# Kernel tuning notes

Measured on AMD Instinct MI355X. Metric: run time of the kernel, lower is better.

Reference implementation:

```python
import jax, jax.numpy as jnp
import numpy as np

APP_DIM = 27
FEA_PE = 6
VIEW_PE = 6
FEATURE_C = 128
DENSITY_SHIFT = -10.0
DISTANCE_SCALE = 25.0
IN_MLPC = 2 * VIEW_PE * 3 + 2 * FEA_PE * APP_DIM + 3 + APP_DIM  # 390


def positional_encoding(x, freqs):
    # x: [..., C] -> [..., 2*freqs*C]
    freq_bands = (2.0 ** jnp.arange(freqs)).astype(x.dtype)
    pts = (x[..., None] * freq_bands).reshape(x.shape[:-1] + (freqs * x.shape[-1],))
    return jnp.concatenate([jnp.sin(pts), jnp.cos(pts)], axis=-1)


def alpha2weights(alpha):
    # alpha: [N_rays, N_samples]; last sample forced opaque (as in source)
    alpha = alpha.at[:, -1].set(1.0)
    trans = jnp.concatenate(
        [jnp.ones((alpha.shape[0], 1), alpha.dtype), 1.0 - alpha + 1e-10], axis=-1)
    T = jnp.cumprod(trans, axis=-1)
    weights = alpha * T[:, :-1]
    return weights, T


def setup_inputs() -> dict:
    key = jax.random.key(0)
    ks = jax.random.split(key, 12)
    N_rays, N_samples = 4096, 128
    sigma_feat = jax.random.normal(ks[0], (N_rays, N_samples), jnp.float32)
    app_features = 0.1 * jax.random.normal(ks[1], (N_rays, N_samples, APP_DIM), jnp.float32)
    vd = jax.random.normal(ks[2], (N_rays, N_samples, 3), jnp.float32)
    viewdirs = vd / (jnp.linalg.norm(vd, axis=-1, keepdims=True) + 1e-8)
    dists = 0.02 * jax.random.uniform(ks[3], (N_rays, N_samples), jnp.float32)

    def linear(k, fan_in, fan_out):
        kw, kb = jax.random.split(k)
        lim = 1.0 / np.sqrt(fan_in)
        W = jax.random.uniform(kw, (fan_in, fan_out), jnp.float32, -lim, lim)
        b = jax.random.uniform(kb, (fan_out,), jnp.float32, -lim, lim)
        return W, b

    W1, b1 = linear(ks[4], IN_MLPC, FEATURE_C)
    W2, b2 = linear(ks[5], FEATURE_C, FEATURE_C)
    W3, _ = linear(ks[6], FEATURE_C, 3)
    b3 = jnp.zeros((3,), jnp.float32)  # bias of last layer initialized to 0 in source
    return {"sigma_feat": sigma_feat, "app_features": app_features,
            "viewdirs": viewdirs, "dists": dists,
            "W1": W1, "b1": b1, "W2": W2, "b2": b2, "W3": W3, "b3": b3}


def reference(sigma_feat, app_features, viewdirs, dists, W1, b1, W2, b2, W3, b3):
    # feature2density: softplus with density_shift
    sigma = jax.nn.softplus(sigma_feat + DENSITY_SHIFT)
    alpha = 1.0 - jnp.exp(-sigma * dists * DISTANCE_SCALE)  # [N_rays, N_samples]
    weights, _T = alpha2weights(alpha)

    # MLPRender_Fea: cat[features, viewdirs, PE(features), PE(viewdirs)]
    mlp_in = jnp.concatenate(
        [app_features, viewdirs,
         positional_encoding(app_features, FEA_PE),
         positional_encoding(viewdirs, VIEW_PE)], axis=-1)  # [R, S, 390]
    h = jax.nn.relu(jnp.einsum('rsc,cf->rsf', mlp_in, W1) + b1)
    h = jax.nn.relu(jnp.einsum('rsf,fg->rsg', h, W2) + b2)
    rgb = jax.nn.sigmoid(jnp.einsum('rsg,go->rso', h, W3) + b3)  # [R, S, 3]

    rgb_map = jnp.sum(weights[..., None] * rgb, axis=-2)  # [R, 3]
    return rgb_map
```

## Files before the change

kernel.cpp:

```cpp
#include <hip/hip_runtime.h>
#include <math.h>

typedef unsigned short u16;
using bf16x8 = __attribute__((ext_vector_type(8))) short;
using f32x4  = __attribute__((ext_vector_type(4))) float;

#define NS      128
#define NBLOCKS 4096
#define NSLICE  19

#define POOLSZ 32768
#define OH2    16384

#define BAR() do { asm volatile("s_waitcnt lgkmcnt(0)" ::: "memory");        \
                   __builtin_amdgcn_s_barrier();                              \
                   asm volatile("" ::: "memory"); } while (0)

#define MF(A,B,C) __builtin_amdgcn_mfma_f32_16x16x32_bf16((A),(B),(C),0,0,0)

__device__ __forceinline__ u16 f2bf(float f) {
    unsigned int i = __float_as_uint(f);
    return (u16)((i + 0x7FFFu + ((i >> 16) & 1u)) >> 16);
}

__device__ __forceinline__ unsigned pk(float hi, float lo) {
    unsigned r;
    asm("v_cvt_pk_bf16_f32 %0, %1, %2" : "=v"(r) : "v"(lo), "v"(hi));
    return r;
}

__device__ __forceinline__ int afoff_h(int m, int k) {
    int chunk = ((k >> 5) * 8 + (m >> 4)) * 64 + ((k >> 3) & 3) * 16 + (m & 15);
    chunk ^= (k >> 3) & 3;
    return chunk * 8 + (k & 7);
}

__device__ __forceinline__ int orig_k(int ch, int slot) {
    if (ch < 27) {
        if (slot == 0) return ch;
        if (slot <= 6) return 30 + ch * 6 + (slot - 1);
        return 192 + ch * 6 + (slot - 7);
    } else {
        int c = ch - 27;
        if (slot == 0) return 27 + c;
        if (slot <= 6) return 354 + c * 6 + (slot - 1);
        return 372 + c * 6 + (slot - 7);
    }
}

__device__ __forceinline__ float ldch(const float* ap, const float* vp, int c) {
    return (c < 27) ? ap[c] : vp[c - 27];
}

__device__ __forceinline__ void build_x(u16* dst, float v) {
    float rev = v * 0.15915494309189535f;
    rev -= floorf(rev);
    float s0 = __builtin_amdgcn_sinf(rev);
    float c0 = __builtin_amdgcn_cosf(rev);
    float s1 = 2.f * s0 * c0, c1 = c0 * c0 - s0 * s0;
    float s2 = 2.f * s1 * c1, c2 = c1 * c1 - s1 * s1;
    float s3 = 2.f * s2 * c2, c3 = c2 * c2 - s2 * s2;
    float s4 = 2.f * s3 * c3, c4 = c3 * c3 - s3 * s3;
    float s5 = 2.f * s4 * c4, c5 = c4 * c4 - s4 * s4;
    uint4 lo, hi;
    lo.x = pk(s0, v);  lo.y = pk(s2, s1);  lo.z = pk(s4, s3);  lo.w = pk(c0, s5);
    hi.x = pk(c2, c1); hi.y = pk(c4, c3);  hi.z = pk(0.f, c5); hi.w = 0u;
    *(uint4*)(dst)       = lo;
    *(uint4*)(dst + 128) = hi;
}

__global__ __launch_bounds__(256) void prep_kernel(
    const float* __restrict__ W1, const float* __restrict__ W2,
    const float* __restrict__ W3, u16* __restrict__ ws,
    float* __restrict__ out)
{
    int idx = blockIdx.x * 256 + threadIdx.x;
    if (idx < 12288) out[idx] = 0.f;
    if (idx < 61440) {
        int j = idx & 7, lane = (idx >> 3) & 63, nt = (idx >> 9) & 7, ks = idx >> 12;
        int q = lane >> 4, l15 = lane & 15;
        int klocal = q * 8 + j;
        int ch = ks * 2 + (klocal >> 4);
        int slot = klocal & 15;
        int n = nt * 16 + l15;
        ws[idx] = (slot < 13) ? f2bf(W1[orig_k(ch, slot) * 128 + n]) : (u16)0;
    } else if (idx < 77824) {
        int i2 = idx - 61440;
        int j = i2 & 7, lane = (i2 >> 3) & 63, nt = (i2 >> 9) & 7, ks = i2 >> 12;
        int k = ks * 32 + (lane >> 4) * 8 + j;
        int n = nt * 16 + (lane & 15);
        ws[idx] = f2bf(W2[k * 128 + n]);
    } else if (idx < 79872) {
        int i3 = idx - 77824;
        int j = i3 & 7, lane = (i3 >> 3) & 63, ks = i3 >> 9;
        int k = ks * 32 + (lane >> 4) * 8 + j;
        int n = lane & 15;
        ws[idx] = (n < 3) ? f2bf(W3[k * 3 + n]) : (u16)0;
    }
}

#define LOADB2(N0, N1, s)                                                     \
    if ((s) < NSLICE) {                                                       \
        const u16* wp = wp0 + (s) * 4096;                                     \
        N0 = *(const bf16x8*)(wp);                                            \
        N1 = *(const bf16x8*)(wp + 512);                                      \
    }

#define BODYX(s, C0,C1, N0,N1)                                                \
  {                                                                           \
    LOADB2(N0, N1, (s)+2);                                                    \
    const u16* ab = pool + ((s)&7)*4096 + (wm*256 + lane)*8;                  \
    bf16x8 a0 = *(const bf16x8*)(ab);                                         \
    bf16x8 a1 = *(const bf16x8*)(ab + 512);                                   \
    __builtin_amdgcn_s_setprio(1);                                            \
    acc[0][0]=MF(a0,C0,acc[0][0]); acc[0][1]=MF(a0,C1,acc[0][1]);             \
    acc[1][0]=MF(a1,C0,acc[1][0]); acc[1][1]=MF(a1,C1,acc[1][1]);             \
    a0 = *(const bf16x8*)(ab + 1024);                                         \
    a1 = *(const bf16x8*)(ab + 1536);                                         \
    acc[2][0]=MF(a0,C0,acc[2][0]); acc[2][1]=MF(a0,C1,acc[2][1]);             \
    acc[3][0]=MF(a1,C0,acc[3][0]); acc[3][1]=MF(a1,C1,acc[3][1]);             \
    __builtin_amdgcn_s_setprio(0);                                            \
  }

#define BODYX0(s, C0,C1, N0,N1)                                               \
  {                                                                           \
    LOADB2(N0, N1, (s)+2);                                                    \
    const u16* ab = pool + ((s)&7)*4096 + (wm*256 + lane)*8;                  \
    bf16x8 a0 = *(const bf16x8*)(ab);                                         \
    bf16x8 a1 = *(const bf16x8*)(ab + 512);                                   \
    __builtin_amdgcn_s_setprio(1);                                            \
    acc[0][0]=MF(a0,C0,vzero); acc[0][1]=MF(a0,C1,vzero);                     \
    acc[1][0]=MF(a1,C0,vzero); acc[1][1]=MF(a1,C1,vzero);                     \
    a0 = *(const bf16x8*)(ab + 1024);                                         \
    a1 = *(const bf16x8*)(ab + 1536);                                         \
    acc[2][0]=MF(a0,C0,vzero); acc[2][1]=MF(a0,C1,vzero);                     \
    acc[3][0]=MF(a1,C0,vzero); acc[3][1]=MF(a1,C1,vzero);                     \
    __builtin_amdgcn_s_setprio(0);                                            \
  }

#define BODYH(s, C0,C1, N0,N1)                                                \
  {                                                                           \
    LOADB2(N0, N1, (s)+2);                                                    \
    int cb = ((((s)-15)*512) + wm*256 + lane) ^ quad;                         \
    bf16x8 a0 = *(const bf16x8*)(pool + cb*8);                                \
    bf16x8 a1 = *(const bf16x8*)(pool + (cb+64)*8);                           \
    __builtin_amdgcn_s_setprio(1);                                            \
    acc[0][0]=MF(a0,C0,acc[0][0]); acc[0][1]=MF(a0,C1,acc[0][1]);             \
    acc[1][0]=MF(a1,C0,acc[1][0]); acc[1][1]=MF(a1,C1,acc[1][1]);             \
    a0 = *(const bf16x8*)(pool + (cb+128)*8);                                 \
    a1 = *(const bf16x8*)(pool + (cb+192)*8);                                 \
    acc[2][0]=MF(a0,C0,acc[2][0]); acc[2][1]=MF(a0,C1,acc[2][1]);             \
    acc[3][0]=MF(a1,C0,acc[3][0]); acc[3][1]=MF(a1,C1,acc[3][1]);             \
    __builtin_amdgcn_s_setprio(0);                                            \
  }

#define BODYH0(s, C0,C1, N0,N1)                                               \
  {                                                                           \
    LOADB2(N0, N1, (s)+2);                                                    \
    int cb = ((((s)-15)*512) + wm*256 + lane) ^ quad;                         \
    bf16x8 a0 = *(const bf16x8*)(pool + cb*8);                                \
    bf16x8 a1 = *(const bf16x8*)(pool + (cb+64)*8);                           \
    __builtin_amdgcn_s_setprio(1);                                            \
    acc[0][0]=MF(a0,C0,vzero); acc[0][1]=MF(a0,C1,vzero);                     \
    acc[1][0]=MF(a1,C0,vzero); acc[1][1]=MF(a1,C1,vzero);                     \
    a0 = *(const bf16x8*)(pool + (cb+128)*8);                                 \
    a1 = *(const bf16x8*)(pool + (cb+192)*8);                                 \
    acc[2][0]=MF(a0,C0,vzero); acc[2][1]=MF(a0,C1,vzero);                     \
    acc[3][0]=MF(a1,C0,vzero); acc[3][1]=MF(a1,C1,vzero);                     \
    __builtin_amdgcn_s_setprio(0);                                            \
  }

#define GENDQ(p)                                                              \
  {                                                                           \
    if (8*(p)+8  + cl < 30)                                                   \
        build_x(pool + ((2*(p)+2)&3)*8192 + (cl>>1)*4096 + bxoff, pv_a);      \
    if (8*(p)+12 + cl < 30)                                                   \
        build_x(pool + ((2*(p)+3)&3)*8192 + (cl>>1)*4096 + bxoff, pv_b);      \
    pv_a = pv_c; pv_b = pv_d;                                                 \
    if (8*(p)+24 + cl < 30) pv_c = ldch(ap, vp, 8*(p)+24 + cl);               \
    if (8*(p)+28 + cl < 30) pv_d = ldch(ap, vp, 8*(p)+28 + cl);               \
    BAR();                                                                    \
  }

#define EPI4(OFS, ACC, BB, rwb, col)                                          \
  { f32x4 t_ = ACC + BB;                                                      \
    t_ = __builtin_elementwise_max(t_, vzero);                                \
    unsigned w01_ = pk(t_[1], t_[0]);                                         \
    unsigned w23_ = pk(t_[3], t_[2]);                                         \
    pool[(OFS) + afoff_h((rwb) + 0, col)] = (u16)w01_;                        \
    pool[(OFS) + afoff_h((rwb) + 1, col)] = (u16)(w01_ >> 16);                \
    pool[(OFS) + afoff_h((rwb) + 2, col)] = (u16)w23_;                        \
    pool[(OFS) + afoff_h((rwb) + 3, col)] = (u16)(w23_ >> 16); }

__global__ __launch_bounds__(512, 4) void render_kernel(
    const float* __restrict__ sigma_g, const float* __restrict__ app_g,
    const float* __restrict__ view_g,  const float* __restrict__ dists_g,
    const float* __restrict__ b1_g,    const float* __restrict__ b2_g,
    const float* __restrict__ b3_g,    const u16* __restrict__ ws,
    float* __restrict__ out_g)
{
    __shared__ __align__(16) u16 pool[POOLSZ];
    __shared__ __align__(16) float part[NS * 3];
    __shared__ float scanS;

    const int tid  = threadIdx.x;
    const int lane = tid & 63;
    const int wave = tid >> 6;
    const int l15  = lane & 15;
    const int quad = lane >> 4;
    const int wm   = wave >> 2;
    const int wn   = wave & 3;

    const int r  = blockIdx.x;
    const int rb = r * NS;
    const int row = tid & 127;
    const int cl  = tid >> 7;
    const float* ap = app_g  + (rb + row) * 27;
    const float* vp = view_g + (rb + row) * 3;
    const int bxoff = (row >> 4) * 512 + (((cl & 1) * 32) + (row & 15)) * 8;

    const u16* wp0 = ws + (wn * 128 + lane) * 8;
    bf16x8 bP0, bP1, bQ0, bQ1, bR0, bR1;
    LOADB2(bP0, bP1, 0);
    LOADB2(bQ0, bQ1, 1);

    float pv_a = ldch(ap, vp, cl);
    float pv_b = ldch(ap, vp, 4 + cl);
    float pv_c = ldch(ap, vp, 8 + cl);
    float pv_d = ldch(ap, vp, 12 + cl);

    float alpha = 0.f, prod = 1.f, wr = 0.f;
    if (tid < NS) {
        float x  = sigma_g[rb + tid] - 10.f;
        float sp = (x > 20.f) ? x : log1pf(expf(x));
        alpha = 1.f - expf(-sp * dists_g[rb + tid] * 25.f);
        if (tid == NS - 1) alpha = 1.f;
        float tb = 1.f - alpha + 1e-10f;
        prod = tb;
        #pragma unroll
        for (int d = 1; d < 64; d <<= 1) {
            float v = __shfl_up(prod, d);
            if (lane >= d) prod *= v;
        }
        if (tid == 63) scanS = prod;
    }

    build_x(pool +        (cl >> 1) * 4096 + bxoff, pv_a);
    build_x(pool + 8192 + (cl >> 1) * 4096 + bxoff, pv_b);
    pv_a = pv_c; pv_b = pv_d;
    pv_c = ldch(ap, vp, 16 + cl);
    pv_d = ldch(ap, vp, 20 + cl);
    BAR();

    if (tid < NS) {
        float prev = __shfl_up(prod, 1);
        float base = (lane == 0) ? 1.f : prev;
        float scale = (wave == 1) ? scanS : 1.f;
        wr = alpha * base * scale;
    }

    const f32x4 vzero = {0.f, 0.f, 0.f, 0.f};
    f32x4 acc[4][2];

    BODYX0(0, bP0,bP1, bR0,bR1);
    BODYX(1,  bQ0,bQ1, bP0,bP1);
    BODYX(2,  bR0,bR1, bQ0,bQ1);
    BODYX(3,  bP0,bP1, bR0,bR1);  GENDQ(0);
    BODYX(4,  bQ0,bQ1, bP0,bP1);
    BODYX(5,  bR0,bR1, bQ0,bQ1);
    BODYX(6,  bP0,bP1, bR0,bR1);
    BODYX(7,  bQ0,bQ1, bP0,bP1);  GENDQ(1);
    BODYX(8,  bR0,bR1, bQ0,bQ1);
    BODYX(9,  bP0,bP1, bR0,bR1);
    BODYX(10, bQ0,bQ1, bP0,bP1);
    BODYX(11, bR0,bR1, bQ0,bQ1);  GENDQ(2);
    const float b1r0 = b1_g[wn * 32 + l15];
    const float b1r1 = b1_g[wn * 32 + 16 + l15];
    BODYX(12, bP0,bP1, bR0,bR1);
    BODYX(13, bQ0,bQ1, bP0,bP1);
    BODYX(14, bR0,bR1, bQ0,bQ1);

    {
        const f32x4 bb0 = {b1r0, b1r0, b1r0, b1r0};
        const f32x4 bb1 = {b1r1, b1r1, b1r1, b1r1};
        #pragma unroll
        for (int mt = 0; mt < 4; ++mt) {
            int rwb = wm * 64 + mt * 16 + quad * 4;
            EPI4(0, acc[mt][0], bb0, rwb, wn * 32 + l15);
            EPI4(0, acc[mt][1], bb1, rwb, wn * 32 + 16 + l15);
        }
    }
    BAR();

    const float b2r0 = b2_g[wn * 32 + l15];
    const float b2r1 = b2_g[wn * 32 + 16 + l15];

    BODYH0(15, bP0,bP1, bR0,bR1);
    BODYH(16, bQ0,bQ1, bP0,bP1);
    BODYH(17, bR0,bR1, bQ0,bQ1);
    BODYH(18, bP0,bP1, bR0,bR1);

    {
        const f32x4 bb0 = {b2r0, b2r0, b2r0, b2r0};
        const f32x4 bb1 = {b2r1, b2r1, b2r1, b2r1};
        #pragma unroll
        for (int mt = 0; mt < 4; ++mt) {
            int rwb = wm * 64 + mt * 16 + quad * 4;
            EPI4(OH2, acc[mt][0], bb0, rwb, wn * 32 + l15);
            EPI4(OH2, acc[mt][1], bb1, rwb, wn * 32 + 16 + l15);
        }
    }
    BAR();

    const u16* w3r = ws + 77824;
    const float b3v = (l15 < 3) ? b3_g[l15] : 0.f;
    f32x4 acc3 = vzero;
    #pragma unroll
    for (int ks = 0; ks < 4; ++ks) {
        bf16x8 w3f = *(const bf16x8*)(w3r + (ks * 64 + lane) * 8);
        int c = ((ks * 8 + wave) * 64 + lane) ^ quad;
        bf16x8 a3 = *(const bf16x8*)(pool + OH2 + c * 8);
        acc3 = MF(a3, w3f, acc3);
    }
    if (l15 < 3) {
        #pragma unroll
        for (int rr = 0; rr < 4; ++rr) {
            int rw = wave * 16 + quad * 4 + rr;
            float v = acc3[rr] + b3v;
            part[rw * 3 + l15] = 1.f / (1.f + expf(-v));
        }
    }
    BAR();

    if (tid < NS) {
        float v0 = wr * part[tid * 3 + 0];
        float v1 = wr * part[tid * 3 + 1];
        float v2 = wr * part[tid * 3 + 2];
        #pragma unroll
        for (int d = 1; d < 64; d <<= 1) {
            v0 += __shfl_xor(v0, d);
            v1 += __shfl_xor(v1, d);
            v2 += __shfl_xor(v2, d);
        }
        if (lane == 0) {
            atomicAdd(&out_g[r * 3 + 0], v0);
            atomicAdd(&out_g[r * 3 + 1], v1);
            atomicAdd(&out_g[r * 3 + 2], v2);
        }
    }
}

extern "C" void kernel_launch(void* const* d_in, const int* in_sizes, int n_in,
                              void* d_out, int out_size, void* d_ws, size_t ws_size,
                              hipStream_t stream) {
    (void)in_sizes; (void)n_in; (void)out_size; (void)ws_size;
    const float* sigma = (const float*)d_in[0];
    const float* app   = (const float*)d_in[1];
    const float* view  = (const float*)d_in[2];
    const float* dists = (const float*)d_in[3];
    const float* W1    = (const float*)d_in[4];
    const float* b1    = (const float*)d_in[5];
    const float* W2    = (const float*)d_in[6];
    const float* b2    = (const float*)d_in[7];
    const float* W3    = (const float*)d_in[8];
    const float* b3    = (const float*)d_in[9];
    float* out = (float*)d_out;

    u16* ws = (u16*)d_ws;

    prep_kernel<<<312, 256, 0, stream>>>(W1, W2, W3, ws, out);
    render_kernel<<<NBLOCKS, 512, 0, stream>>>(sigma, app, view, dists,
                                               b1, b2, b3, ws, out);
}
```

Measured before the change: 196.3 us.

## Precompute ray sample weights in prep kernel and reduce per-wave with atomics

The softplus/alpha/transmittance scan moves out of the render kernel into the prep kernel, which writes per-sample weights to the workspace. The render kernel then loads four weights per lane and applies sigmoid and weighting directly on the MFMA accumulators. Each wave reduces with two xor-shuffles and issues its own atomics, which removes the shared `part` buffer, the `scanS` scan state and one block barrier at the tail. In exchange, each ray now takes eight times as many global atomics, and the prep kernel grows to 1024 blocks and adds a weight-buffer round trip through global memory.

```diff
diff --git a/kernel.cpp b/kernel.cpp
--- a/kernel.cpp
+++ b/kernel.cpp
@@ -8,6 +8,7 @@
 #define NS      128
 #define NBLOCKS 4096
 #define NSLICE  19
+#define OWGT    81920
 
 #define POOLSZ 32768
 #define OH2    16384
@@ -71,7 +72,8 @@
 
 __global__ __launch_bounds__(256) void prep_kernel(
     const float* __restrict__ W1, const float* __restrict__ W2,
-    const float* __restrict__ W3, u16* __restrict__ ws,
+    const float* __restrict__ W3, const float* __restrict__ sigma_g,
+    const float* __restrict__ dists_g, u16* __restrict__ ws,
     float* __restrict__ out)
 {
     int idx = blockIdx.x * 256 + threadIdx.x;
@@ -97,6 +99,31 @@
         int n = lane & 15;
         ws[idx] = (n < 3) ? f2bf(W3[k * 3 + n]) : (u16)0;
     }
+    {
+        int ray = idx >> 6, ln = idx & 63;
+        float* wgt = (float*)(ws + OWGT);
+        int base = ray * NS;
+        float x0 = sigma_g[base + ln] - 10.f;
+        float sp0 = (x0 > 20.f) ? x0 : log1pf(expf(x0));
+        float a0 = 1.f - expf(-sp0 * dists_g[base + ln] * 25.f);
+        float x1 = sigma_g[base + 64 + ln] - 10.f;
+        float sp1 = (x1 > 20.f) ? x1 : log1pf(expf(x1));
+        float a1 = 1.f - expf(-sp1 * dists_g[base + 64 + ln] * 25.f);
+        if (ln == 63) a1 = 1.f;
+        float p0 = 1.f - a0 + 1e-10f;
+        float p1 = 1.f - a1 + 1e-10f;
+        #pragma unroll
+        for (int d = 1; d < 64; d <<= 1) {
+            float v0 = __shfl_up(p0, d);
+            float v1 = __shfl_up(p1, d);
+            if (ln >= d) { p0 *= v0; p1 *= v1; }
+        }
+        float S0 = __shfl(p0, 63);
+        float q0 = __shfl_up(p0, 1);
+        float q1 = __shfl_up(p1, 1);
+        wgt[base + ln]      = a0 * ((ln == 0) ? 1.f : q0);
+        wgt[base + 64 + ln] = a1 * ((ln == 0) ? 1.f : q1) * S0;
+    }
 }
 
 #define LOADB2(N0, N1, s)                                                     \
@@ -193,15 +220,12 @@
     pool[(OFS) + afoff_h((rwb) + 3, col)] = (u16)(w23_ >> 16); }
 
 __global__ __launch_bounds__(512, 4) void render_kernel(
-    const float* __restrict__ sigma_g, const float* __restrict__ app_g,
-    const float* __restrict__ view_g,  const float* __restrict__ dists_g,
+    const float* __restrict__ app_g,   const float* __restrict__ view_g,
     const float* __restrict__ b1_g,    const float* __restrict__ b2_g,
     const float* __restrict__ b3_g,    const u16* __restrict__ ws,
     float* __restrict__ out_g)
 {
     __shared__ __align__(16) u16 pool[POOLSZ];
-    __shared__ __align__(16) float part[NS * 3];
-    __shared__ float scanS;
 
     const int tid  = threadIdx.x;
     const int lane = tid & 63;
@@ -229,35 +253,12 @@
     float pv_c = ldch(ap, vp, 8 + cl);
     float pv_d = ldch(ap, vp, 12 + cl);
 
-    float alpha = 0.f, prod = 1.f, wr = 0.f;
-    if (tid < NS) {
-        float x  = sigma_g[rb + tid] - 10.f;
-        float sp = (x > 20.f) ? x : log1pf(expf(x));
-        alpha = 1.f - expf(-sp * dists_g[rb + tid] * 25.f);
-        if (tid == NS - 1) alpha = 1.f;
-        float tb = 1.f - alpha + 1e-10f;
-        prod = tb;
-        #pragma unroll
-        for (int d = 1; d < 64; d <<= 1) {
-            float v = __shfl_up(prod, d);
-            if (lane >= d) prod *= v;
-        }
-        if (tid == 63) scanS = prod;
-    }
-
     build_x(pool +        (cl >> 1) * 4096 + bxoff, pv_a);
     build_x(pool + 8192 + (cl >> 1) * 4096 + bxoff, pv_b);
     pv_a = pv_c; pv_b = pv_d;
     pv_c = ldch(ap, vp, 16 + cl);
     pv_d = ldch(ap, vp, 20 + cl);
     BAR();
-
-    if (tid < NS) {
-        float prev = __shfl_up(prod, 1);
-        float base = (lane == 0) ? 1.f : prev;
-        float scale = (wave == 1) ? scanS : 1.f;
-        wr = alpha * base * scale;
-    }
 
     const f32x4 vzero = {0.f, 0.f, 0.f, 0.f};
     f32x4 acc[4][2];
@@ -313,6 +314,8 @@
     BAR();
 
     const u16* w3r = ws + 77824;
+    const float4 w4 = *(const float4*)((const float*)(ws + OWGT)
+                                       + rb + wave * 16 + quad * 4);
     const float b3v = (l15 < 3) ? b3_g[l15] : 0.f;
     f32x4 acc3 = vzero;
     #pragma unroll
@@ -322,32 +325,17 @@
         bf16x8 a3 = *(const bf16x8*)(pool + OH2 + c * 8);
         acc3 = MF(a3, w3f, acc3);
     }
+    float v = 0.f;
     if (l15 < 3) {
-        #pragma unroll
-        for (int rr = 0; rr < 4; ++rr) {
-            int rw = wave * 16 + quad * 4 + rr;
-            float v = acc3[rr] + b3v;
-            part[rw * 3 + l15] = 1.f / (1.f + expf(-v));
-        }
-    }
-    BAR();
-
-    if (tid < NS) {
-        float v0 = wr * part[tid * 3 + 0];
-        float v1 = wr * part[tid * 3 + 1];
-        float v2 = wr * part[tid * 3 + 2];
-        #pragma unroll
-        for (int d = 1; d < 64; d <<= 1) {
-            v0 += __shfl_xor(v0, d);
-            v1 += __shfl_xor(v1, d);
-            v2 += __shfl_xor(v2, d);
-        }
-        if (lane == 0) {
-            atomicAdd(&out_g[r * 3 + 0], v0);
-            atomicAdd(&out_g[r * 3 + 1], v1);
-            atomicAdd(&out_g[r * 3 + 2], v2);
-        }
-    }
+        v  = w4.x / (1.f + expf(-(acc3[0] + b3v)));
+        v += w4.y / (1.f + expf(-(acc3[1] + b3v)));
+        v += w4.z / (1.f + expf(-(acc3[2] + b3v)));
+        v += w4.w / (1.f + expf(-(acc3[3] + b3v)));
+    }
+    v += __shfl_xor(v, 16);
+    v += __shfl_xor(v, 32);
+    if (lane < 3)
+        atomicAdd(&out_g[r * 3 + lane], v);
 }
 
 extern "C" void kernel_launch(void* const* d_in, const int* in_sizes, int n_in,
@@ -368,7 +356,6 @@
 
     u16* ws = (u16*)d_ws;
 
-    prep_kernel<<<312, 256, 0, stream>>>(W1, W2, W3, ws, out);
-    render_kernel<<<NBLOCKS, 512, 0, stream>>>(sigma, app, view, dists,
-                                               b1, b2, b3, ws, out);
-}
+    prep_kernel<<<1024, 256, 0, stream>>>(W1, W2, W3, sigma, dists, ws, out);
+    render_kernel<<<NBLOCKS, 512, 0, stream>>>(app, view, b1, b2, b3, ws, out);
+}
```

After: 192.9 us (median of 2 runs). Within noise of the previous version (-1.7%).
